# Performance work log

Hardware: AMD Instinct MI355X
Metric: run time of the kernel (lower is better)

The kernel has to match this reference:

```python
import jax, jax.numpy as jnp
import numpy as np
import math

KH, KW = 3, 3
CIN, COUT = 48, 48
H, W = 128, 128
DELTA = 0.001


def _gabor_weights(freq, theta, sigma, psi, f0, theta0):
    # grids exactly as in torch __init__: x0 = ceil(kh/2), linspace(-x0+1, x0, kh)
    x0 = math.ceil(KH / 2)
    y0 = math.ceil(KW / 2)
    ly = jnp.linspace(-x0 + 1.0, float(x0), KH)
    lx = jnp.linspace(-y0 + 1.0, float(y0), KW)
    Y, X = jnp.meshgrid(ly, lx, indexing='ij')  # [kh,kw], Y varies on dim0
    # broadcast per-(out,in) scalars over the kernel grid -> [O,I,kh,kw]
    th = theta[:, :, None, None]
    sg = sigma[:, :, None, None]
    fr = freq[:, :, None, None]
    ps = psi[:, :, None, None]
    F0 = f0[:, :, None, None]
    th0 = theta0[:, :, None, None]
    rotx = X * jnp.cos(th) + Y * jnp.sin(th)
    roty = -X * jnp.sin(th) + Y * jnp.cos(th)
    r = jnp.sqrt(rotx ** 2 + roty ** 2 + DELTA)
    g_radial = jnp.exp(-((jnp.log(r) - jnp.log(F0)) / (2.0 * jnp.log(sg / F0))) ** 2)
    g_angular = jnp.exp(-(th - th0) ** 2 / (2.0 * sg ** 2))
    g = g_radial * g_angular * jnp.cos(fr * r + ps)
    g = g / (2.0 * math.pi * sg ** 2)
    return g  # [O,I,KH,KW]


def setup_inputs() -> dict:
    key = jax.random.key(0)
    ks = jax.random.split(key, 5)
    pi = math.pi
    return {
        'x': jax.random.normal(ks[0], (1, CIN, H, W), dtype=jnp.float32),
        'freq': jax.random.uniform(ks[1], (COUT, CIN), dtype=jnp.float32) * pi,
        'theta': jax.random.uniform(ks[2], (COUT, CIN), dtype=jnp.float32) * pi,
        'sigma': jax.random.uniform(ks[3], (COUT, CIN), dtype=jnp.float32) * pi,
        'psi': jax.random.uniform(ks[4], (COUT, CIN), dtype=jnp.float32) * pi,
        'f0': jnp.ones((COUT, CIN), dtype=jnp.float32),
        'theta0': jnp.ones((COUT, CIN), dtype=jnp.float32),
    }


def reference(x, freq, theta, sigma, psi, f0, theta0):
    w = _gabor_weights(freq, theta, sigma, psi, f0, theta0)  # [O,I,kh,kw]
    # frequency-domain filtering: fft2(x) [1,I,H,W] * fft2(w, s=(H,W)) [O,I,H,W]
    x_freq = jnp.fft.fft2(x)
    w_freq = jnp.fft.fft2(w, s=(H, W))
    xf = x_freq * w_freq  # broadcast (B=1) -> [O,I,H,W]
    crow, ccol = H // 2, W // 2
    mask = jnp.zeros((H, W), dtype=x.dtype).at[crow - 30:crow + 30, ccol - 30:ccol + 30].set(1.0)
    x_filtered = jnp.fft.ifft2(xf * mask).real  # [O,I,H,W]
    out = jax.lax.conv_general_dilated(
        x_filtered, w,
        window_strides=(1, 1), padding=[(1, 1), (1, 1)],
        dimension_numbers=('NCHW', 'OIHW', 'NCHW'))
    return out  # [O,O,H,W]
```

## Files before the change

### kernel.cpp

```cpp
#include <hip/hip_runtime.h>

#define CIN 48
#define COUT 48
#define NPIX 16384
#define XFP 52

typedef float f32x4 __attribute__((ext_vector_type(4)));
typedef short bf16x8 __attribute__((ext_vector_type(8)));

__device__ __forceinline__ unsigned short f2bf(float f) {
  unsigned u = __float_as_uint(f);
  unsigned r = (u + 0x7FFFu + ((u >> 16) & 1u)) >> 16;
  return (unsigned short)r;
}

__global__ __launch_bounds__(256) void gabor_k(
    const float* __restrict__ freq, const float* __restrict__ theta,
    const float* __restrict__ sigma, const float* __restrict__ psi,
    const float* __restrict__ f0, const float* __restrict__ theta0,
    float* __restrict__ wout, unsigned short* __restrict__ wbf64)
{
  int idx = blockIdx.x * 256 + threadIdx.x;
  if (idx < 432 * 16) {
    wbf64[(idx >> 4) * 64 + 48 + (idx & 15)] = 0;
  }
  if (idx >= COUT * CIN * 9) return;
  int k = idx % 9;
  int oi = idx / 9;
  int oc = oi / CIN, ic = oi % CIN;
  int a = k / 3, b = k % 3;
  float Yv = (a == 0) ? -1.0f : ((a == 1) ? 0.5f : 2.0f);
  float Xv = (b == 0) ? -1.0f : ((b == 1) ? 0.5f : 2.0f);
  float th = theta[oi], sg = sigma[oi], fr = freq[oi], ps = psi[oi];
  float F0 = f0[oi], th0 = theta0[oi];
  float c = cosf(th), s = sinf(th);
  float rotx =  Xv * c + Yv * s;
  float roty = -Xv * s + Yv * c;
  float r = sqrtf(rotx * rotx + roty * roty + 0.001f);
  float denom = 2.0f * logf(sg / F0);
  float t1 = (logf(r) - logf(F0)) / denom;
  float g_rad = expf(-t1 * t1);
  float dth = th - th0;
  float g_ang = expf(-dth * dth / (2.0f * sg * sg));
  float g = g_rad * g_ang * cosf(fr * r + ps) / (6.283185307179586f * sg * sg);
  wout[idx] = g;
  wbf64[(k * 48 + oc) * 64 + ic] = f2bf(g);
}

__global__ void circ_k(float* __restrict__ ar, float* __restrict__ ai)
{
  int d = threadIdx.x;
  float sr = 0.f, si = 0.f;
  for (int u = 34; u < 94; ++u) {
    int m = (u * d) & 127;
    float ang = (float)m * 0.049087385212340526f;
    sr += cosf(ang);
    si += sinf(ang);
  }
  ar[d] = sr * (1.0f / 128.0f);
  ai[d] = si * (1.0f / 128.0f);
}

__global__ __launch_bounds__(256) void stage1_k(
    const float* __restrict__ x, const float* __restrict__ arr,
    const float* __restrict__ aii, float2* __restrict__ Up)
{
  __shared__ float Xs[16 * 128];
  __shared__ float ars[128], ais[128];
  int yg = blockIdx.x, i = blockIdx.y;
  int t = threadIdx.x;
  const float* Xi = x + i * NPIX + yg * 16 * 128;
  for (int p = t; p < 2048; p += 256) Xs[p] = Xi[p];
  if (t < 128) { ars[t] = arr[t]; ais[t] = aii[t]; }
  __syncthreads();
  int j = t & 127;
  int ysl = t >> 7;
  float accr[8], acci[8];
#pragma unroll
  for (int yy = 0; yy < 8; ++yy) { accr[yy] = 0.f; acci[yy] = 0.f; }
  for (int xx = 0; xx < 128; ++xx) {
    float tr = ars[(j - xx) & 127];
    float ti = ais[(j - xx) & 127];
#pragma unroll
    for (int yy = 0; yy < 8; ++yy) {
      float xv = Xs[(ysl * 8 + yy) * 128 + xx];
      accr[yy] += xv * tr;
      acci[yy] += xv * ti;
    }
  }
  float2* UpI = Up + i * NPIX;
  int ybase = yg * 16 + ysl * 8;
#pragma unroll
  for (int yy = 0; yy < 8; ++yy)
    UpI[(ybase + yy) * 128 + j] = make_float2(accr[yy], acci[yy]);
}

__global__ __launch_bounds__(256) void stage2_k(
    const float2* __restrict__ Up, const float* __restrict__ arr,
    const float* __restrict__ aii, float* __restrict__ yf)
{
  __shared__ float2 Us[128 * 16];
  __shared__ float ars[128], ais[128];
  int jg = blockIdx.x, i = blockIdx.y;
  int t = threadIdx.x;
  const float2* UpI = Up + i * NPIX;
  for (int p = t; p < 2048; p += 256) {
    int y = p >> 4, jj = p & 15;
    Us[p] = UpI[y * 128 + jg * 16 + jj];
  }
  if (t < 128) { ars[t] = arr[t]; ais[t] = aii[t]; }
  __syncthreads();
  int yp = t & 127;
  int xsl = t >> 7;
  float acc[8];
#pragma unroll
  for (int xx = 0; xx < 8; ++xx) acc[xx] = 0.f;
  for (int y = 0; y < 128; ++y) {
    float tr = ars[(yp - y) & 127];
    float ti = ais[(yp - y) & 127];
#pragma unroll
    for (int xx = 0; xx < 8; ++xx) {
      float2 u = Us[y * 16 + xsl * 8 + xx];
      acc[xx] += u.x * tr - u.y * ti;
    }
  }
  float* yfI = yf + i * NPIX;
  int xb = jg * 16 + xsl * 8;
#pragma unroll
  for (int xx = 0; xx < 8; ++xx)
    yfI[yp * 128 + xb + xx] = acc[xx];
}

__global__ __launch_bounds__(256, 3) void conv2_k(
    const float* __restrict__ yf, const float* __restrict__ wts,
    const unsigned short* __restrict__ wbf64, float* __restrict__ out)
{
  __shared__ __align__(16) short XF[324 * XFP + 16];

  int o  = blockIdx.z;
  int y0 = blockIdx.y * 16, x0 = blockIdx.x * 16;
  int tid = threadIdx.x;

  for (int p = tid; p < 324; p += 256)
    *(uint2*)(XF + p * XFP + 48) = make_uint2(0u, 0u);
  if (tid < 16) XF[324 * XFP + tid] = 0;

  if (tid < 240) {
    int sA = tid, sB = tid + 240;
    int iA = sA / 10, rA = sA - iA * 10, spA = rA % 5, hA = rA / 5;
    int iB = sB / 10, rB = sB - iB * 10, spB = rB % 5, hB = rB / 5;
    const float* WpA = wts + (o * CIN + iA) * 9;
    const float* WpB = wts + (o * CIN + iB) * 9;
    float WA0 = WpA[0], WA1 = WpA[1], WA2 = WpA[2], WA3 = WpA[3], WA4 = WpA[4],
          WA5 = WpA[5], WA6 = WpA[6], WA7 = WpA[7], WA8 = WpA[8];
    float WB0 = WpB[0], WB1 = WpB[1], WB2 = WpB[2], WB3 = WpB[3], WB4 = WpB[4],
          WB5 = WpB[5], WB6 = WpB[6], WB7 = WpB[7], WB8 = WpB[8];
    const float* yfA = yf + iA * NPIX;
    const float* yfB = yf + iB * NPIX;
    int cbA = (x0 - 4 + 4 * spA) & 127;
    int cbB = (x0 - 4 + 4 * spB) & 127;
    int rbA = hA * 9, rbB = hB * 9;
    float RaA[8], RbA[8], RcA[8], RaB[8], RbB[8], RcB[8];

#define LOADA(dst, ry) { \
    const float* rp_ = yfA + (((ry) & 127) << 7); \
    float4 q0_ = *(const float4*)(rp_ + cbA); \
    float4 q1_ = *(const float4*)(rp_ + ((cbA + 4) & 127)); \
    dst[0]=q0_.x; dst[1]=q0_.y; dst[2]=q0_.z; dst[3]=q0_.w; \
    dst[4]=q1_.x; dst[5]=q1_.y; dst[6]=q1_.z; dst[7]=q1_.w; }
#define LOADB(dst, ry) { \
    const float* rp_ = yfB + (((ry) & 127) << 7); \
    float4 q0_ = *(const float4*)(rp_ + cbB); \
    float4 q1_ = *(const float4*)(rp_ + ((cbB + 4) & 127)); \
    dst[0]=q0_.x; dst[1]=q0_.y; dst[2]=q0_.z; dst[3]=q0_.w; \
    dst[4]=q1_.x; dst[5]=q1_.y; dst[6]=q1_.z; dst[7]=q1_.w; }

#define EMITA(rr, R2_, R1_, R0_) { \
    int y_ = y0 - 1 + (rr); \
    bool yok_ = (y_ >= 0) && (y_ < 128); \
    _Pragma("unroll") \
    for (int j = 0; j < 4; ++j) { \
      int cidx_ = 4 * spA + j; \
      if (cidx_ < 18) { \
        int xg_ = x0 - 1 + cidx_; \
        float v_ = 0.f; \
        if (yok_ && xg_ >= 0 && xg_ < 128) { \
          v_ = WA0 * R0_[j + 3] + WA1 * R0_[j + 2] + WA2 * R0_[j + 1] \
             + WA3 * R1_[j + 3] + WA4 * R1_[j + 2] + WA5 * R1_[j + 1] \
             + WA6 * R2_[j + 3] + WA7 * R2_[j + 2] + WA8 * R2_[j + 1]; \
        } \
        XF[((rr) * 18 + cidx_) * XFP + iA] = (short)f2bf(v_); \
      } } }
#define EMITB(rr, R2_, R1_, R0_) { \
    int y_ = y0 - 1 + (rr); \
    bool yok_ = (y_ >= 0) && (y_ < 128); \
    _Pragma("unroll") \
    for (int j = 0; j < 4; ++j) { \
      int cidx_ = 4 * spB + j; \
      if (cidx_ < 18) { \
        int xg_ = x0 - 1 + cidx_; \
        float v_ = 0.f; \
        if (yok_ && xg_ >= 0 && xg_ < 128) { \
          v_ = WB0 * R0_[j + 3] + WB1 * R0_[j + 2] + WB2 * R0_[j + 1] \
             + WB3 * R1_[j + 3] + WB4 * R1_[j + 2] + WB5 * R1_[j + 1] \
             + WB6 * R2_[j + 3] + WB7 * R2_[j + 2] + WB8 * R2_[j + 1]; \
        } \
        XF[((rr) * 18 + cidx_) * XFP + iB] = (short)f2bf(v_); \
      } } }

    LOADA(RaA, y0 - 3 + rbA)  LOADB(RaB, y0 - 3 + rbB)
    LOADA(RbA, y0 - 2 + rbA)  LOADB(RbB, y0 - 2 + rbB)
#pragma unroll
    for (int rr0 = 0; rr0 < 9; rr0 += 3) {
      LOADA(RcA, y0 - 1 + rbA + rr0)  LOADB(RcB, y0 - 1 + rbB + rr0)
      EMITA(rbA + rr0,     RaA, RbA, RcA)  EMITB(rbB + rr0,     RaB, RbB, RcB)
      LOADA(RaA, y0 + rbA + rr0)      LOADB(RaB, y0 + rbB + rr0)
      EMITA(rbA + rr0 + 1, RbA, RcA, RaA)  EMITB(rbB + rr0 + 1, RbB, RcB, RaB)
      LOADA(RbA, y0 + 1 + rbA + rr0)  LOADB(RbB, y0 + 1 + rbB + rr0)
      EMITA(rbA + rr0 + 2, RcA, RaA, RbA)  EMITB(rbB + rr0 + 2, RcB, RaB, RbB)
    }
#undef LOADA
#undef LOADB
#undef EMITA
#undef EMITB
  }
  __syncthreads();

  int wv = tid >> 6, lane = tid & 63;
  int tx = lane & 15, gq = lane >> 4;
  f32x4 acc[4][3];
#pragma unroll
  for (int nn = 0; nn < 4; ++nn)
#pragma unroll
    for (int m = 0; m < 3; ++m) acc[nn][m] = (f32x4){0.f, 0.f, 0.f, 0.f};

  const unsigned short* abase = wbf64 + (tx)*64;

  for (int k = 0; k < 9; ++k) {
    bf16x8 Ac0[3], Ac1[3];
#pragma unroll
    for (int m = 0; m < 3; ++m) {
      const unsigned short* ap = abase + (k * 48 + m * 16) * 64;
      Ac0[m] = *(const bf16x8*)(ap + gq * 8);
      Ac1[m] = *(const bf16x8*)(ap + 32 + gq * 8);
    }
    int dy = k / 3, dx = k - dy * 3;
#pragma unroll
    for (int nn = 0; nn < 4; ++nn) {
      int n = wv * 4 + nn;
      const short* bp = XF + ((n + dy) * 18 + tx + dx) * XFP;
      bf16x8 B0 = *(const bf16x8*)(bp + gq * 8);
      bf16x8 B1 = *(const bf16x8*)(bp + 32 + gq * 8);
#pragma unroll
      for (int m = 0; m < 3; ++m) {
        acc[nn][m] = __builtin_amdgcn_mfma_f32_16x16x32_bf16(Ac0[m], B0, acc[nn][m], 0, 0, 0);
        acc[nn][m] = __builtin_amdgcn_mfma_f32_16x16x32_bf16(Ac1[m], B1, acc[nn][m], 0, 0, 0);
      }
    }
  }

#pragma unroll
  for (int nn = 0; nn < 4; ++nn) {
    int y = y0 + wv * 4 + nn;
#pragma unroll
    for (int m = 0; m < 3; ++m) {
#pragma unroll
      for (int r = 0; r < 4; ++r) {
        int oc = m * 16 + gq * 4 + r;
        out[((size_t)(o * COUT + oc) << 14) + (y << 7) + x0 + tx] = acc[nn][m][r];
      }
    }
  }
}

extern "C" void kernel_launch(void* const* d_in, const int* in_sizes, int n_in,
                              void* d_out, int out_size, void* d_ws, size_t ws_size,
                              hipStream_t stream)
{
  const float* x      = (const float*)d_in[0];
  const float* freq   = (const float*)d_in[1];
  const float* theta  = (const float*)d_in[2];
  const float* sigma  = (const float*)d_in[3];
  const float* psi    = (const float*)d_in[4];
  const float* f0     = (const float*)d_in[5];
  const float* theta0 = (const float*)d_in[6];
  float* out = (float*)d_out;
  float* ws  = (float*)d_ws;

  float*  w   = ws;
  float*  ar  = ws + 20736;
  float*  ai  = ws + 20864;
  float2* Up  = (float2*)(ws + 21248);
  float*  yf  = ws + 21248 + CIN * NPIX * 2;
  unsigned short* wbf64 = (unsigned short*)(ws + 21248 + CIN * NPIX * 3);

  gabor_k<<<dim3(81), dim3(256), 0, stream>>>(freq, theta, sigma, psi, f0, theta0, w, wbf64);
  circ_k<<<dim3(1), dim3(128), 0, stream>>>(ar, ai);
  stage1_k<<<dim3(8, 48), dim3(256), 0, stream>>>(x, ar, ai, Up);
  stage2_k<<<dim3(8, 48), dim3(256), 0, stream>>>(Up, ar, ai, yf);
  conv2_k<<<dim3(8, 8, 48), dim3(256), 0, stream>>>(yf, w, wbf64, out);
}
```

Measured before the change: 174.2 us.

## Split conv stage: MFMA stage computes depthwise-filtered maps, then gathered conv

Adds a path, used when the workspace is large enough, that precomputes the per-(o,i) 3x3 filtered images (the first conv with the Gabor weights) as a small MFMA GEMM. It uses split bf16 hi/lo weights and activations to keep precision, and writes a bf16 intermediate tensor of size 48x48x16384. A new conv2g kernel then loads this intermediate directly into LDS instead of recomputing the 9-tap stencil per tile in scalar FP32. The aim is to move the scalar stencil work onto matrix cores, at the cost of roughly 220 MB of extra global write and read traffic.

```diff
diff --git a/kernel.cpp b/kernel.cpp
--- a/kernel.cpp
+++ b/kernel.cpp
@@ -13,16 +13,31 @@
   unsigned r = (u + 0x7FFFu + ((u >> 16) & 1u)) >> 16;
   return (unsigned short)r;
 }
+__device__ __forceinline__ float bf2f(unsigned short b) {
+  return __uint_as_float(((unsigned)b) << 16);
+}
+
+#define OFF_UP     21248
+#define OFF_YF     (OFF_UP + CIN * NPIX * 2)
+#define OFF_WBF64  (OFF_YF + CIN * NPIX)
+#define OFF_WSPLIT (OFF_WBF64 + 13824)
+#define OFF_XFG    (OFF_WSPLIT + 73728)
+#define WS_NEEDED  ((size_t)(OFF_XFG + 48 * 48 * NPIX / 2) * 4)
 
 __global__ __launch_bounds__(256) void gabor_k(
     const float* __restrict__ freq, const float* __restrict__ theta,
     const float* __restrict__ sigma, const float* __restrict__ psi,
     const float* __restrict__ f0, const float* __restrict__ theta0,
-    float* __restrict__ wout, unsigned short* __restrict__ wbf64)
+    float* __restrict__ wout, unsigned short* __restrict__ wbf64,
+    unsigned int* __restrict__ wsplitU, int big)
 {
   int idx = blockIdx.x * 256 + threadIdx.x;
   if (idx < 432 * 16) {
     wbf64[(idx >> 4) * 64 + 48 + (idx & 15)] = 0;
+  }
+  if (big && idx < 2304 * 14) {
+    int row = idx / 14, q = idx - row * 14;
+    wsplitU[row * 32 + 18 + q] = 0u;
   }
   if (idx >= COUT * CIN * 9) return;
   int k = idx % 9;
@@ -45,6 +60,15 @@
   float g = g_rad * g_ang * cosf(fr * r + ps) / (6.283185307179586f * sg * sg);
   wout[idx] = g;
   wbf64[(k * 48 + oc) * 64 + ic] = f2bf(g);
+  if (big) {
+    unsigned short w0 = f2bf(g);
+    unsigned short w1 = f2bf(g - bf2f(w0));
+    unsigned int u0 = (unsigned)w0 | ((unsigned)w0 << 16);
+    unsigned int u1 = (unsigned)w1 | ((unsigned)w1 << 16);
+    unsigned int* rowp = wsplitU + (ic * 48 + oc) * 32;
+    rowp[k * 2]     = u0;
+    rowp[k * 2 + 1] = u1;
+  }
 }
 
 __global__ void circ_k(float* __restrict__ ar, float* __restrict__ ai)
@@ -129,6 +153,169 @@
 #pragma unroll
   for (int xx = 0; xx < 8; ++xx)
     yfI[yp * 128 + xb + xx] = acc[xx];
+}
+
+__global__ __launch_bounds__(256, 3) void stageA_k(
+    const float* __restrict__ yf, const unsigned short* __restrict__ wsplit,
+    unsigned short* __restrict__ xfg)
+{
+  __shared__ unsigned int bpU[512];
+  __shared__ __align__(16) unsigned int BU[256 * 34];
+  int Y0 = blockIdx.x * 2, i = blockIdx.y;
+  int tid = threadIdx.x;
+  const float* yfi = yf + i * NPIX;
+
+  for (int j = tid; j < 512; j += 256) {
+    int r = j >> 7, cx = j & 127;
+    int gy = (Y0 - 2 + r) & 127;
+    float v = yfi[gy * 128 + cx];
+    unsigned short b0 = f2bf(v);
+    unsigned short b1 = f2bf(v - bf2f(b0));
+    bpU[j] = (unsigned)b0 | ((unsigned)b1 << 16);
+  }
+  __syncthreads();
+
+  {
+    int px = tid;
+    int ry = px >> 7, xx = px & 127;
+    unsigned int* brow = BU + px * 34;
+#pragma unroll
+    for (int k = 0; k < 9; ++k) {
+      int dy = k / 3, dx = k - dy * 3;
+      int r = 2 + ry - dy;
+      int c = (xx - dx) & 127;
+      unsigned int pr = bpU[r * 128 + c];
+      brow[2 * k] = pr;
+      brow[2 * k + 1] = pr;
+    }
+#pragma unroll
+    for (int q = 18; q < 34; ++q) brow[q] = 0u;
+  }
+  __syncthreads();
+
+  int wv = tid >> 6, lane = tid & 63;
+  int tx = lane & 15, gq = lane >> 4;
+  f32x4 acc[4][3];
+#pragma unroll
+  for (int nn = 0; nn < 4; ++nn)
+#pragma unroll
+    for (int m = 0; m < 3; ++m) acc[nn][m] = (f32x4){0.f, 0.f, 0.f, 0.f};
+
+  const unsigned short* wsA = wsplit + i * (48 * 64);
+#pragma unroll
+  for (int half = 0; half < 2; ++half) {
+    bf16x8 Af[3];
+#pragma unroll
+    for (int m = 0; m < 3; ++m)
+      Af[m] = *(const bf16x8*)(wsA + (m * 16 + tx) * 64 + half * 32 + gq * 8);
+#pragma unroll
+    for (int nn = 0; nn < 4; ++nn) {
+      int px = (wv * 4 + nn) * 16 + tx;
+      bf16x8 Bf = *(const bf16x8*)((const short*)BU + px * 68 + half * 32 + gq * 8);
+#pragma unroll
+      for (int m = 0; m < 3; ++m)
+        acc[nn][m] = __builtin_amdgcn_mfma_f32_16x16x32_bf16(Af[m], Bf, acc[nn][m], 0, 0, 0);
+    }
+  }
+
+#pragma unroll
+  for (int nn = 0; nn < 4; ++nn) {
+    int p = Y0 * 128 + (wv * 4 + nn) * 16 + tx;
+#pragma unroll
+    for (int m = 0; m < 3; ++m) {
+#pragma unroll
+      for (int r = 0; r < 4; ++r) {
+        int o = m * 16 + gq * 4 + r;
+        xfg[((size_t)(o * 48 + i) << 14) + p] = f2bf(acc[nn][m][r]);
+      }
+    }
+  }
+}
+
+__global__ __launch_bounds__(256, 3) void conv2g_k(
+    const unsigned short* __restrict__ xfg,
+    const unsigned short* __restrict__ wbf64, float* __restrict__ out)
+{
+  __shared__ __align__(16) short XF[324 * XFP + 16];
+
+  int o  = blockIdx.z;
+  int y0 = blockIdx.y * 16, x0 = blockIdx.x * 16;
+  int tid = threadIdx.x;
+
+  for (int p = tid; p < 324; p += 256)
+    *(uint2*)(XF + p * XFP + 48) = make_uint2(0u, 0u);
+  if (tid < 16) XF[324 * XFP + tid] = 0;
+
+  for (int task = tid; task < 864; task += 256) {
+    int i = task % 48, rr = task / 48;
+    int y = y0 - 1 + rr;
+    short* dst = XF + rr * 18 * XFP + i;
+    if (y >= 0 && y < 128) {
+      const unsigned short* src = xfg + ((size_t)(o * 48 + i) << 14) + (y << 7);
+      uint4 qa = *(const uint4*)(src + x0);
+      uint4 qb = *(const uint4*)(src + x0 + 8);
+      unsigned short e0  = (x0 > 0)        ? src[x0 - 1]  : (unsigned short)0;
+      unsigned short e17 = (x0 + 16 < 128) ? src[x0 + 16] : (unsigned short)0;
+      unsigned int qs[8] = {qa.x, qa.y, qa.z, qa.w, qb.x, qb.y, qb.z, qb.w};
+      dst[0] = (short)e0;
+#pragma unroll
+      for (int h = 0; h < 8; ++h) {
+        dst[(2 * h + 1) * XFP] = (short)(qs[h] & 0xffffu);
+        dst[(2 * h + 2) * XFP] = (short)(qs[h] >> 16);
+      }
+      dst[17 * XFP] = (short)e17;
+    } else {
+#pragma unroll
+      for (int c = 0; c < 18; ++c) dst[c * XFP] = 0;
+    }
+  }
+  __syncthreads();
+
+  int wv = tid >> 6, lane = tid & 63;
+  int tx = lane & 15, gq = lane >> 4;
+  f32x4 acc[4][3];
+#pragma unroll
+  for (int nn = 0; nn < 4; ++nn)
+#pragma unroll
+    for (int m = 0; m < 3; ++m) acc[nn][m] = (f32x4){0.f, 0.f, 0.f, 0.f};
+
+  const unsigned short* abase = wbf64 + (tx)*64;
+
+  for (int k = 0; k < 9; ++k) {
+    bf16x8 Ac0[3], Ac1[3];
+#pragma unroll
+    for (int m = 0; m < 3; ++m) {
+      const unsigned short* ap = abase + (k * 48 + m * 16) * 64;
+      Ac0[m] = *(const bf16x8*)(ap + gq * 8);
+      Ac1[m] = *(const bf16x8*)(ap + 32 + gq * 8);
+    }
+    int dy = k / 3, dx = k - dy * 3;
+#pragma unroll
+    for (int nn = 0; nn < 4; ++nn) {
+      int n = wv * 4 + nn;
+      const short* bp = XF + ((n + dy) * 18 + tx + dx) * XFP;
+      bf16x8 B0 = *(const bf16x8*)(bp + gq * 8);
+      bf16x8 B1 = *(const bf16x8*)(bp + 32 + gq * 8);
+#pragma unroll
+      for (int m = 0; m < 3; ++m) {
+        acc[nn][m] = __builtin_amdgcn_mfma_f32_16x16x32_bf16(Ac0[m], B0, acc[nn][m], 0, 0, 0);
+        acc[nn][m] = __builtin_amdgcn_mfma_f32_16x16x32_bf16(Ac1[m], B1, acc[nn][m], 0, 0, 0);
+      }
+    }
+  }
+
+#pragma unroll
+  for (int nn = 0; nn < 4; ++nn) {
+    int y = y0 + wv * 4 + nn;
+#pragma unroll
+    for (int m = 0; m < 3; ++m) {
+#pragma unroll
+      for (int r = 0; r < 4; ++r) {
+        int oc = m * 16 + gq * 4 + r;
+        out[((size_t)(o * COUT + oc) << 14) + (y << 7) + x0 + tx] = acc[nn][m][r];
+      }
+    }
+  }
 }
 
 __global__ __launch_bounds__(256, 3) void conv2_k(
@@ -174,7 +361,6 @@
     float4 q1_ = *(const float4*)(rp_ + ((cbB + 4) & 127)); \
     dst[0]=q0_.x; dst[1]=q0_.y; dst[2]=q0_.z; dst[3]=q0_.w; \
     dst[4]=q1_.x; dst[5]=q1_.y; dst[6]=q1_.z; dst[7]=q1_.w; }
-
 #define EMITA(rr, R2_, R1_, R0_) { \
     int y_ = y0 - 1 + (rr); \
     bool yok_ = (y_ >= 0) && (y_ < 128); \
@@ -287,16 +473,26 @@
   float* out = (float*)d_out;
   float* ws  = (float*)d_ws;
 
-  float*  w   = ws;
-  float*  ar  = ws + 20736;
-  float*  ai  = ws + 20864;
-  float2* Up  = (float2*)(ws + 21248);
-  float*  yf  = ws + 21248 + CIN * NPIX * 2;
-  unsigned short* wbf64 = (unsigned short*)(ws + 21248 + CIN * NPIX * 3);
-
-  gabor_k<<<dim3(81), dim3(256), 0, stream>>>(freq, theta, sigma, psi, f0, theta0, w, wbf64);
+  float*  w      = ws;
+  float*  ar     = ws + 20736;
+  float*  ai     = ws + 20864;
+  float2* Up     = (float2*)(ws + OFF_UP);
+  float*  yf     = ws + OFF_YF;
+  unsigned short* wbf64  = (unsigned short*)(ws + OFF_WBF64);
+  unsigned int*   wsplit = (unsigned int*)(ws + OFF_WSPLIT);
+  unsigned short* xfg    = (unsigned short*)(ws + OFF_XFG);
+
+  int big = (ws_size >= WS_NEEDED) ? 1 : 0;
+
+  gabor_k<<<dim3(126), dim3(256), 0, stream>>>(freq, theta, sigma, psi, f0, theta0,
+                                               w, wbf64, wsplit, big);
   circ_k<<<dim3(1), dim3(128), 0, stream>>>(ar, ai);
   stage1_k<<<dim3(8, 48), dim3(256), 0, stream>>>(x, ar, ai, Up);
   stage2_k<<<dim3(8, 48), dim3(256), 0, stream>>>(Up, ar, ai, yf);
-  conv2_k<<<dim3(8, 8, 48), dim3(256), 0, stream>>>(yf, w, wbf64, out);
-}
+  if (big) {
+    stageA_k<<<dim3(64, 48), dim3(256), 0, stream>>>(yf, (const unsigned short*)wsplit, xfg);
+    conv2g_k<<<dim3(8, 8, 48), dim3(256), 0, stream>>>(xfg, wbf64, out);
+  } else {
+    conv2_k<<<dim3(8, 8, 48), dim3(256), 0, stream>>>(yf, w, wbf64, out);
+  }
+}
```

After: 230.5 us. 1.32x slower.
